# Kernel optimization log

Measured on AMD Instinct MI355X. Metric: run time of the kernel, lower is better.

Reference implementation:

```python
import jax, jax.numpy as jnp
import numpy as np

B, N, C = 8, 4096, 768
H, M = 12, 64          # num_heads, num_landmarks
D = C // H             # head_dim = 64


def setup_inputs() -> dict:
    key = jax.random.key(0)
    k1, k2, k3, k4 = jax.random.split(key, 4)
    s = 0.02
    return {
        "x": jax.random.normal(k1, (B, N, C), dtype=jnp.float32),
        "w_qkv": jax.random.normal(k2, (3 * C, C), dtype=jnp.float32) * s,
        "w_proj": jax.random.normal(k3, (C, C), dtype=jnp.float32) * s,
        "b_proj": jax.random.normal(k4, (C,), dtype=jnp.float32) * s,
    }


def iterative_inv(mat, n_iter=6):
    # mat: [B, H, M, M]; Newton-Schulz cubic iteration for pseudo-inverse
    I = jnp.eye(mat.shape[-1], dtype=mat.dtype)
    K = mat
    # init: K^T / max_j(sum_i K_ij)  per (B,H)
    scale = jnp.max(jnp.sum(K, axis=-2), axis=-1)[:, :, None, None]
    V = jnp.swapaxes(K, -1, -2) / scale
    for _ in range(n_iter):
        KV = K @ V
        V = 0.25 * V @ (13.0 * I - KV @ (15.0 * I - KV @ (7.0 * I - KV)))
    return V


def reference(x, w_qkv, w_proj, b_proj):
    b, n, c = x.shape
    qkv = (x @ w_qkv.T).reshape(b, n, 3, H, D).transpose(2, 0, 3, 1, 4)  # [3,B,H,N,D]
    Q, K, V = qkv[0], qkv[1], qkv[2]
    Q = Q / (D ** 0.5)
    # landmark pooling (N % M == 0 path): segment means of length N//M
    Kl = K.reshape(b, H, M, n // M, D).mean(axis=-2)  # [B,H,M,D]
    Ql = Q.reshape(b, H, M, n // M, D).mean(axis=-2)  # [B,H,M,D]
    kernel1 = jax.nn.softmax(jnp.einsum('bhnd,bhmd->bhnm', Q, Kl), axis=-1)   # [B,H,N,M]
    kernel2 = jax.nn.softmax(jnp.einsum('bhmd,bhld->bhml', Ql, Kl), axis=-1)  # [B,H,M,M]
    kernel3 = jax.nn.softmax(jnp.einsum('bhmd,bhnd->bhmn', Ql, K), axis=-1)   # [B,H,M,N]
    SV = (kernel1 @ iterative_inv(kernel2)) @ (kernel3 @ V)  # [B,H,N,D]
    SV = SV.transpose(0, 2, 1, 3).reshape(b, n, c)
    out = SV @ w_proj.T + b_proj
    out = out + V.transpose(0, 2, 1, 3).reshape(b, n, c)
    return out
```

## Files before the change

kernel.cpp:

```cpp
#include <hip/hip_runtime.h>
#include <hip/hip_bf16.h>
#include <stdint.h>

typedef __bf16 bf16;
typedef __bf16 bf16x8 __attribute__((ext_vector_type(8)));
typedef __bf16 bf16x4 __attribute__((ext_vector_type(4)));
typedef float f32x4 __attribute__((ext_vector_type(4)));

#define B_ 8
#define N_ 4096
#define C_ 768
#define H_ 12
#define M_ 64
#define D_ 64
#define NT_ 32768
#define C3_ 2304

typedef __attribute__((address_space(3))) void lds_void_t;
typedef const __attribute__((address_space(1))) void gvoid_t;

__device__ __forceinline__ void gl_lds16(const void* gsrc, void* ldst) {
  __builtin_amdgcn_global_load_lds((gvoid_t*)(uintptr_t)gsrc,
                                   (lds_void_t*)(uintptr_t)ldst, 16, 0, 0);
}

__device__ __forceinline__ f32x4 mfma16(bf16x8 a, bf16x8 b, f32x4 c) {
  return __builtin_amdgcn_mfma_f32_16x16x32_bf16(a, b, c, 0, 0, 0);
}

#define VMW8 asm volatile("s_waitcnt vmcnt(8)" ::: "memory")
#define VMW4 asm volatile("s_waitcnt vmcnt(4)" ::: "memory")
#define VMW0 asm volatile("s_waitcnt vmcnt(0)" ::: "memory")
#define RAWBAR() { __builtin_amdgcn_sched_barrier(0); __builtin_amdgcn_s_barrier(); __builtin_amdgcn_sched_barrier(0); }

__global__ void k_cvt(const float* __restrict__ in, bf16* __restrict__ out, int n4) {
  const int stride = gridDim.x * blockDim.x;
  for (int i = blockIdx.x * blockDim.x + threadIdx.x; i < n4; i += stride) {
    f32x4 v = *(const f32x4*)(in + (size_t)i * 4);
    bf16x4 o;
    o[0] = (bf16)v[0]; o[1] = (bf16)v[1]; o[2] = (bf16)v[2]; o[3] = (bf16)v[3];
    *(bf16x4*)(out + (size_t)i * 4) = o;
  }
}

__global__ __launch_bounds__(512, 2) void k_qkv(
    const bf16* __restrict__ xbf, const bf16* __restrict__ wbf,
    bf16* __restrict__ Qb, bf16* __restrict__ Kb, bf16* __restrict__ Vb,
    float* __restrict__ Qlf, float* __restrict__ Klf)
{
  __shared__ bf16 As[4][8192];
  __shared__ bf16 Bs[4][8192];
  const int t = threadIdx.x;
  const int wave = t >> 6, lane = t & 63;
  const int l15 = lane & 15, l16 = lane >> 4;

  const int bid = blockIdx.x;
  const int swz = (bid & 7) * 144 + (bid >> 3);
  const int bt = swz / 9, ct = swz % 9;
  const int row0 = bt * 256, col0 = ct * 256;
  const int wr = wave >> 2, wc = wave & 3;

  const int srow = t >> 2;
  const int scol = (((t & 3) ^ ((t >> 3) & 3)) << 3);
  const bf16* gaBase = xbf + (size_t)(row0 + srow) * C_ + scol;
  const bf16* gbBase = wbf + (size_t)(col0 + srow) * C_ + scol;

  const int aoff = (wr * 128 + l15) * 32 + ((l16 ^ ((l15 >> 1) & 3)) << 3);
  const int boff = (wc * 64 + l15) * 32 + ((l16 ^ ((l15 >> 1) & 3)) << 3);

  f32x4 acc[8][4] = {};

#define QSTAGE(kt3) {                                                            \
    const int sb_ = (kt3) & 3;                                                   \
    gl_lds16(gaBase + (kt3) * 32, &As[sb_][t * 8]);                              \
    gl_lds16(gbBase + (kt3) * 32, &Bs[sb_][t * 8]);                              \
    gl_lds16(gaBase + (size_t)128 * C_ + (kt3) * 32, &As[sb_][(t + 512) * 8]);   \
    gl_lds16(gbBase + (size_t)128 * C_ + (kt3) * 32, &Bs[sb_][(t + 512) * 8]); }

#define QKSTEP(kt, DO_STAGE, VMW_, DO_SYNC) {                                    \
    const bf16* as_ = As[(kt) & 3];                                              \
    const bf16* bs_ = Bs[(kt) & 3];                                              \
    bf16x8 bfr[4], afr[8];                                                       \
    _Pragma("unroll")                                                            \
    for (int j = 0; j < 4; ++j) bfr[j] = *(const bf16x8*)&bs_[boff + j * 512];   \
    _Pragma("unroll")                                                            \
    for (int i = 0; i < 8; ++i) afr[i] = *(const bf16x8*)&as_[aoff + i * 512];   \
    if (DO_STAGE) QSTAGE((kt) + 3);                                              \
    if (DO_SYNC) RAWBAR();                 \
    __builtin_amdgcn_s_setprio(1);                                               \
    _Pragma("unroll")                                                            \
    for (int i = 0; i < 8; ++i)                                                  \
      _Pragma("unroll")                                                          \
      for (int j = 0; j < 4; ++j)                                                \
        acc[i][j] = mfma16(afr[i], bfr[j], acc[i][j]);                           \
    __builtin_amdgcn_s_setprio(0);                                               \
    if (DO_SYNC) { VMW_; RAWBAR(); } }

  QSTAGE(0); QSTAGE(1); QSTAGE(2);
  VMW8;
  RAWBAR();

#pragma unroll 3
  for (int kt = 0; kt < 21; ++kt) { QKSTEP(kt, 1, VMW8, 1); }
  QKSTEP(21, 0, VMW4, 1);
  QKSTEP(22, 0, VMW0, 1);
  QKSTEP(23, 0, (void)0, 0);

#undef QKSTEP
#undef QSTAGE

  const int colblock = col0 + wc * 64;
  const int which = colblock / C_;
  const int h = (colblock % C_) / D_;
  const int b = row0 >> 12;
  const int n_base = (row0 & (N_ - 1)) + wr * 128;
  bf16* dst = (which == 0) ? Qb : (which == 1) ? Kb : Vb;
  const float scale = (which == 0) ? 0.125f : 1.0f;
  const size_t base = ((size_t)(b * H_ + h) * N_ + n_base) * D_;
#pragma unroll
  for (int i = 0; i < 8; ++i)
#pragma unroll
    for (int q = 0; q < 4; ++q) {
      const int rloc = i * 16 + l16 * 4 + q;
#pragma unroll
      for (int j = 0; j < 4; ++j) {
        const int d = j * 16 + l15;
        dst[base + (size_t)rloc * D_ + d] = (bf16)(acc[i][j][q] * scale);
      }
    }
  if (which < 2) {
    float* lmout = (which == 0) ? Qlf : Klf;
#pragma unroll
    for (int g = 0; g < 2; ++g) {
      const int m = (n_base >> 6) + g;
#pragma unroll
      for (int j = 0; j < 4; ++j) {
        float s = 0.f;
#pragma unroll
        for (int i = 4 * g; i < 4 * g + 4; ++i)
#pragma unroll
          for (int q = 0; q < 4; ++q) s += acc[i][j][q];
        s *= scale;
        s += __shfl_xor(s, 16);
        s += __shfl_xor(s, 32);
        if (l16 == 0)
          lmout[((size_t)(b * H_ + h) * M_ + m) * D_ + j * 16 + lane] = s * (1.0f / 64.0f);
      }
    }
  }
}

__global__ __launch_bounds__(512, 1) void k_inv(
    const float* __restrict__ Qlf, const float* __restrict__ Klf,
    float* __restrict__ pinv, bf16* __restrict__ Qlb, bf16* __restrict__ Klb)
{
  __shared__ float K2[4096];
  __shared__ float Vm[4096];
  __shared__ float KV[4096];
  __shared__ float T1[4096];
  __shared__ float U1[4096];
  __shared__ float tmp64[64];
  __shared__ float sscale;
  const int t = threadIdx.x;
  const int bh = blockIdx.x;
  const size_t off = (size_t)bh * 4096;
  for (int idx = t; idx < 4096; idx += 512) {
    const float q = Qlf[off + idx];
    T1[idx] = q;
    Qlb[off + idx] = (bf16)q;
  }
  for (int idx = t; idx < 4096; idx += 512) {
    const int r = idx >> 6, c = idx & 63;
    const float k = Klf[off + idx];
    U1[c * 64 + r] = k;
    Klb[off + idx] = (bf16)k;
  }
  __syncthreads();
  const int j0 = (t & 15) * 4;
  const int i0 = (t >> 4) * 2;

  auto MMstep = [&](const float* A, const float* Bm, float* O, float dg, float sg, float al) {
    float r2[2][4] = {};
    for (int k = 0; k < 64; ++k) {
      f32x4 bv = *(const f32x4*)&Bm[k * 64 + j0];
      const float a0 = A[(i0 + 0) * 64 + k];
      const float a1 = A[(i0 + 1) * 64 + k];
#pragma unroll
      for (int jj = 0; jj < 4; ++jj) { r2[0][jj] += a0 * bv[jj]; r2[1][jj] += a1 * bv[jj]; }
    }
#pragma unroll
    for (int ii = 0; ii < 2; ++ii)
#pragma unroll
      for (int jj = 0; jj < 4; ++jj)
        O[(i0 + ii) * 64 + j0 + jj] = al * (dg * A[(i0 + ii) * 64 + (j0 + jj)] + sg * r2[ii][jj]);
    __syncthreads();
  };

  {
    float r2[2][4] = {};
    for (int k = 0; k < 64; ++k) {
      f32x4 bv = *(const f32x4*)&U1[k * 64 + j0];
      const float a0 = T1[(i0 + 0) * 64 + k];
      const float a1 = T1[(i0 + 1) * 64 + k];
#pragma unroll
      for (int jj = 0; jj < 4; ++jj) { r2[0][jj] += a0 * bv[jj]; r2[1][jj] += a1 * bv[jj]; }
    }
#pragma unroll
    for (int ii = 0; ii < 2; ++ii)
#pragma unroll
      for (int jj = 0; jj < 4; ++jj)
        K2[(i0 + ii) * 64 + j0 + jj] = __expf(r2[ii][jj]);
  }
  __syncthreads();
  if (t < 64) {
    float s = 0.f;
    for (int k = 0; k < 64; ++k) s += K2[t * 64 + k];
    tmp64[t] = 1.0f / s;
  }
  __syncthreads();
  for (int idx = t; idx < 4096; idx += 512) K2[idx] *= tmp64[idx >> 6];
  __syncthreads();
  if (t < 64) {
    float s = 0.f;
    for (int i = 0; i < 64; ++i) s += K2[i * 64 + t];
    tmp64[t] = s;
  }
  __syncthreads();
  if (t == 0) {
    float mx = tmp64[0];
    for (int j2 = 1; j2 < 64; ++j2) mx = fmaxf(mx, tmp64[j2]);
    sscale = 1.0f / mx;
  }
  __syncthreads();
  for (int idx = t; idx < 4096; idx += 512) {
    const int r = idx >> 6, c = idx & 63;
    Vm[idx] = K2[c * 64 + r] * sscale;
  }
  __syncthreads();

  float* pV = Vm;
  float* pT = T1;
  for (int it = 0; it < 6; ++it) {
    MMstep(K2, pV, KV, 0.f, 1.f, 1.f);
    MMstep(KV, KV, pT, 7.f, -1.f, 1.f);
    MMstep(KV, pT, U1, 15.f, -1.f, 1.f);
    MMstep(pV, U1, pT, 13.f, -1.f, 0.25f);
    float* sw = pV; pV = pT; pT = sw;
  }
  for (int idx = t; idx < 4096; idx += 512) pinv[off + idx] = pV[idx];
}

__global__ __launch_bounds__(256, 2) void k_k3v(
    const bf16* __restrict__ Qlb, const bf16* __restrict__ Kb, const bf16* __restrict__ Vb,
    float* __restrict__ Zacc, float* __restrict__ rowsum_g)
{
  __shared__ bf16 Qls[64 * 64];
  __shared__ bf16 Ks[128 * 64];
  __shared__ bf16 Vs[128 * 64];
  __shared__ bf16 Ps[64 * 128];
  __shared__ float rs[64];
  const int t = threadIdx.x, wave = t >> 6, lane = t & 63;
  const int bh = blockIdx.x >> 3;
  const int chunk = blockIdx.x & 7;
  const size_t kvbase = (size_t)bh * N_ * D_ + (size_t)chunk * 512 * D_;
  {
    const bf16* g = Qlb + (size_t)bh * 4096;
    gl_lds16(g + t * 8, &Qls[t * 8]);
    gl_lds16(g + (t + 256) * 8, &Qls[(t + 256) * 8]);
  }
  if (t < 64) rs[t] = 0.f;
  f32x4 z[4] = {};
  for (int st = 0; st < 4; ++st) {
    const bf16* gk = Kb + kvbase + (size_t)st * 128 * D_;
    const bf16* gv = Vb + kvbase + (size_t)st * 128 * D_;
#pragma unroll
    for (int c = 0; c < 4; ++c) {
      gl_lds16(gk + (t + c * 256) * 8, &Ks[(t + c * 256) * 8]);
      gl_lds16(gv + (t + c * 256) * 8, &Vs[(t + c * 256) * 8]);
    }
    __syncthreads();
    f32x4 sacc[4][2] = {};
#pragma unroll
    for (int kk = 0; kk < 2; ++kk) {
      bf16x8 af[4], bk[2];
#pragma unroll
      for (int i = 0; i < 4; ++i)
        af[i] = *(const bf16x8*)&Qls[(i * 16 + (lane & 15)) * 64 + kk * 32 + 8 * (lane >> 4)];
#pragma unroll
      for (int j2 = 0; j2 < 2; ++j2)
        bk[j2] = *(const bf16x8*)&Ks[(wave * 32 + j2 * 16 + (lane & 15)) * 64 + kk * 32 + 8 * (lane >> 4)];
#pragma unroll
      for (int i = 0; i < 4; ++i)
#pragma unroll
        for (int j2 = 0; j2 < 2; ++j2)
          sacc[i][j2] = mfma16(af[i], bk[j2], sacc[i][j2]);
    }
#pragma unroll
    for (int i = 0; i < 4; ++i)
#pragma unroll
      for (int q = 0; q < 4; ++q) {
        const float e0 = __expf(sacc[i][0][q]);
        const float e1 = __expf(sacc[i][1][q]);
        const int m = i * 16 + (lane >> 4) * 4 + q;
        Ps[m * 128 + wave * 32 + (lane & 15)] = (bf16)e0;
        Ps[m * 128 + wave * 32 + 16 + (lane & 15)] = (bf16)e1;
        float p = e0 + e1;
        p += __shfl_xor(p, 1); p += __shfl_xor(p, 2);
        p += __shfl_xor(p, 4); p += __shfl_xor(p, 8);
        if ((lane & 15) == 0) atomicAdd(&rs[m], p);
      }
    __syncthreads();
#pragma unroll
    for (int kk = 0; kk < 4; ++kk) {
      const int kbase = kk * 32 + 8 * (lane >> 4);
      const int d = wave * 16 + (lane & 15);
      bf16x8 bv;
#pragma unroll
      for (int e = 0; e < 8; ++e) bv[e] = Vs[(kbase + e) * 64 + d];
#pragma unroll
      for (int i = 0; i < 4; ++i) {
        bf16x8 ap = *(const bf16x8*)&Ps[(i * 16 + (lane & 15)) * 128 + kbase];
        z[i] = mfma16(ap, bv, z[i]);
      }
    }
    __syncthreads();
  }
  const size_t zbase = (size_t)bh * 4096;
#pragma unroll
  for (int i = 0; i < 4; ++i)
#pragma unroll
    for (int q = 0; q < 4; ++q) {
      const int m = i * 16 + (lane >> 4) * 4 + q;
      const int d = wave * 16 + (lane & 15);
      atomicAdd(&Zacc[zbase + m * 64 + d], z[i][q]);
    }
  if (t < 64) atomicAdd(&rowsum_g[bh * 64 + t], rs[t]);
}

__global__ __launch_bounds__(256, 1) void k_comb(
    const float* __restrict__ pinv, const float* __restrict__ Zacc,
    const float* __restrict__ rowsum_g, bf16* __restrict__ Wtb)
{
  __shared__ float Pv[4096];
  __shared__ float Zn[4096];
  const int t = threadIdx.x, bh = blockIdx.x;
  const size_t off = (size_t)bh * 4096;
  for (int idx = t; idx < 4096; idx += 256) Pv[idx] = pinv[off + idx];
  for (int idx = t; idx < 4096; idx += 256)
    Zn[idx] = Zacc[off + idx] / rowsum_g[bh * 64 + (idx >> 6)];
  __syncthreads();
  const int j0 = (t & 15) * 4, i0 = (t >> 4) * 4;
  float r[4][4] = {{0.f}};
  for (int k = 0; k < 64; ++k) {
    f32x4 bv = *(const f32x4*)&Zn[k * 64 + j0];
    float a[4];
#pragma unroll
    for (int ii = 0; ii < 4; ++ii) a[ii] = Pv[(i0 + ii) * 64 + k];
#pragma unroll
    for (int ii = 0; ii < 4; ++ii)
#pragma unroll
      for (int jj = 0; jj < 4; ++jj) r[ii][jj] += a[ii] * bv[jj];
  }
#pragma unroll
  for (int ii = 0; ii < 4; ++ii)
#pragma unroll
    for (int jj = 0; jj < 4; ++jj)
      Wtb[off + (size_t)(j0 + jj) * 64 + (i0 + ii)] = (bf16)r[ii][jj];
}

__global__ __launch_bounds__(256, 2) void k_sv(
    const bf16* __restrict__ Qb, const bf16* __restrict__ Klb,
    const bf16* __restrict__ Wtb, bf16* __restrict__ SVb)
{
  __shared__ bf16 Qs[128 * 64];
  __shared__ bf16 Kls[64 * 64];
  __shared__ bf16 Wts[64 * 64];
  __shared__ bf16 Ps[128 * 64];
  const int t = threadIdx.x, wave = t >> 6, lane = t & 63;
  const int bh = blockIdx.x >> 5;
  const int nt = blockIdx.x & 31;
  const int b = bh / H_, h = bh % H_;
  {
    const bf16* gq = Qb + (size_t)bh * N_ * D_ + (size_t)nt * 128 * D_;
#pragma unroll
    for (int c = 0; c < 4; ++c) gl_lds16(gq + (t + c * 256) * 8, &Qs[(t + c * 256) * 8]);
    const bf16* gkl = Klb + (size_t)bh * 4096;
    gl_lds16(gkl + t * 8, &Kls[t * 8]);
    gl_lds16(gkl + (t + 256) * 8, &Kls[(t + 256) * 8]);
    const bf16* gw = Wtb + (size_t)bh * 4096;
    gl_lds16(gw + t * 8, &Wts[t * 8]);
    gl_lds16(gw + (t + 256) * 8, &Wts[(t + 256) * 8]);
  }
  __syncthreads();
  f32x4 sacc[2][4] = {};
#pragma unroll
  for (int kk = 0; kk < 2; ++kk) {
    bf16x8 af[2], bl[4];
#pragma unroll
    for (int r = 0; r < 2; ++r)
      af[r] = *(const bf16x8*)&Qs[(wave * 32 + r * 16 + (lane & 15)) * 64 + kk * 32 + 8 * (lane >> 4)];
#pragma unroll
    for (int j = 0; j < 4; ++j)
      bl[j] = *(const bf16x8*)&Kls[(j * 16 + (lane & 15)) * 64 + kk * 32 + 8 * (lane >> 4)];
#pragma unroll
    for (int r = 0; r < 2; ++r)
#pragma unroll
      for (int j = 0; j < 4; ++j)
        sacc[r][j] = mfma16(af[r], bl[j], sacc[r][j]);
  }
#pragma unroll
  for (int r = 0; r < 2; ++r)
#pragma unroll
    for (int q = 0; q < 4; ++q) {
      float e[4]; float s = 0.f;
#pragma unroll
      for (int j = 0; j < 4; ++j) { e[j] = __expf(sacc[r][j][q]); s += e[j]; }
      s += __shfl_xor(s, 1); s += __shfl_xor(s, 2);
      s += __shfl_xor(s, 4); s += __shfl_xor(s, 8);
      const float is = 1.0f / s;
      const int row = wave * 32 + r * 16 + (lane >> 4) * 4 + q;
#pragma unroll
      for (int j = 0; j < 4; ++j)
        Ps[row * 64 + j * 16 + (lane & 15)] = (bf16)(e[j] * is);
    }
  __syncthreads();
  f32x4 oacc[2][4] = {};
#pragma unroll
  for (int kk = 0; kk < 2; ++kk) {
    bf16x8 af[2], bw[4];
#pragma unroll
    for (int r = 0; r < 2; ++r)
      af[r] = *(const bf16x8*)&Ps[(wave * 32 + r * 16 + (lane & 15)) * 64 + kk * 32 + 8 * (lane >> 4)];
#pragma unroll
    for (int j = 0; j < 4; ++j)
      bw[j] = *(const bf16x8*)&Wts[(j * 16 + (lane & 15)) * 64 + kk * 32 + 8 * (lane >> 4)];
#pragma unroll
    for (int r = 0; r < 2; ++r)
#pragma unroll
      for (int j = 0; j < 4; ++j)
        oacc[r][j] = mfma16(af[r], bw[j], oacc[r][j]);
  }
  const size_t outbase = ((size_t)b * N_ + (size_t)nt * 128) * C_ + h * 64;
#pragma unroll
  for (int r = 0; r < 2; ++r)
#pragma unroll
    for (int q = 0; q < 4; ++q) {
      const int row = wave * 32 + r * 16 + (lane >> 4) * 4 + q;
#pragma unroll
      for (int j = 0; j < 4; ++j)
        SVb[outbase + (size_t)row * C_ + j * 16 + (lane & 15)] = (bf16)(oacc[r][j][q]);
    }
}

__global__ __launch_bounds__(256, 2) void k_proj(
    const bf16* __restrict__ SVb, const bf16* __restrict__ wpb,
    const float* __restrict__ bproj, const bf16* __restrict__ Vb,
    float* __restrict__ outp)
{
  __shared__ bf16 As[4][4096];
  __shared__ bf16 Bs[4][4096];
  const int t = threadIdx.x;
  const int wave = t >> 6, lane = t & 63;
  const int l15 = lane & 15, l16 = lane >> 4;
  const int bid = blockIdx.x;
  const int swz = (bid & 7) * 192 + (bid >> 3);
  const int bt = swz / 6, ct = swz % 6;
  const int row0 = bt * 128, col0 = ct * 128;
  const int wr = wave >> 1, wc = wave & 1;

  const int srow = t >> 2;
  const int scol = (((t & 3) ^ ((t >> 3) & 3)) << 3);
  const bf16* ga = SVb + (size_t)(row0 + srow) * C_ + scol;
  const bf16* gb = wpb + (size_t)(col0 + srow) * C_ + scol;

  const int aoff = (wr * 64 + l15) * 32 + ((l16 ^ ((l15 >> 1) & 3)) << 3);
  const int boff = (wc * 64 + l15) * 32 + ((l16 ^ ((l15 >> 1) & 3)) << 3);

  f32x4 acc[4][4] = {};

#define PSTAGE(kt3) {                                                          \
    const int sb_ = (kt3) & 3;                                                 \
    gl_lds16(ga + (kt3) * 32, &As[sb_][t * 8]);                                \
    gl_lds16(gb + (kt3) * 32, &Bs[sb_][t * 8]);                                \
    gl_lds16(ga + (size_t)64 * C_ + (kt3) * 32, &As[sb_][(t + 256) * 8]);      \
    gl_lds16(gb + (size_t)64 * C_ + (kt3) * 32, &Bs[sb_][(t + 256) * 8]); }

#define PKSTEP(kt, DO_STAGE, VMW_, DO_SYNC) {                                  \
    const bf16* as_ = As[(kt) & 3];                                            \
    const bf16* bs_ = Bs[(kt) & 3];                                            \
    bf16x8 afr[4], bfr[4];                                                     \
    _Pragma("unroll")                                                          \
    for (int j = 0; j < 4; ++j) bfr[j] = *(const bf16x8*)&bs_[boff + j * 512]; \
    _Pragma("unroll")                                                          \
    for (int i = 0; i < 4; ++i) afr[i] = *(const bf16x8*)&as_[aoff + i * 512]; \
    if (DO_STAGE) PSTAGE((kt) + 3);                                            \
    if (DO_SYNC) RAWBAR();                                                     \
    __builtin_amdgcn_s_setprio(1);                                             \
    _Pragma("unroll")                                                          \
    for (int i = 0; i < 4; ++i)                                                \
      _Pragma("unroll")                                                        \
      for (int j = 0; j < 4; ++j)                                              \
        acc[i][j] = mfma16(afr[i], bfr[j], acc[i][j]);                         \
    __builtin_amdgcn_s_setprio(0);                                             \
    if (DO_SYNC) { VMW_; RAWBAR(); } }

  PSTAGE(0); PSTAGE(1); PSTAGE(2);
  VMW8;
  RAWBAR();

#pragma unroll 3
  for (int kt = 0; kt < 21; ++kt) { PKSTEP(kt, 1, VMW8, 1); }
  PKSTEP(21, 0, VMW4, 1);
  PKSTEP(22, 0, VMW0, 1);
  PKSTEP(23, 0, (void)0, 0);

#undef PKSTEP
#undef PSTAGE

#pragma unroll
  for (int i = 0; i < 4; ++i)
#pragma unroll
    for (int q = 0; q < 4; ++q) {
      const int row = row0 + wr * 64 + i * 16 + l16 * 4 + q;
      const int b = row >> 12, n = row & (N_ - 1);
#pragma unroll
      for (int j = 0; j < 4; ++j) {
        const int col = col0 + wc * 64 + j * 16 + l15;
        const int h = col >> 6, d = col & 63;
        const float v = acc[i][j][q] + bproj[col] +
                        (float)Vb[((size_t)(b * H_ + h) * N_ + n) * D_ + d];
        outp[(size_t)row * C_ + col] = v;
      }
    }
}

extern "C" void kernel_launch(void* const* d_in, const int* in_sizes, int n_in,
                              void* d_out, int out_size, void* d_ws, size_t ws_size,
                              hipStream_t stream) {
  const float* x = (const float*)d_in[0];
  const float* wqkv = (const float*)d_in[1];
  const float* wproj = (const float*)d_in[2];
  const float* bproj = (const float*)d_in[3];
  float* outp = (float*)d_out;
  char* ws = (char*)d_ws;

  size_t off = 0;
  auto take = [&](size_t bytes) { char* p = ws + off; off += bytes; return p; };
  bf16* xbf     = (bf16*)take(50331648);
  bf16* wqkvbf  = (bf16*)take(3538944);
  bf16* wprojbf = (bf16*)take(1179648);
  bf16* Qb      = (bf16*)take(50331648);
  bf16* Kb      = (bf16*)take(50331648);
  bf16* Vb      = (bf16*)take(50331648);
  float* Qlf    = (float*)take(1572864);
  float* Klf    = (float*)take(1572864);
  bf16* Qlb     = (bf16*)take(786432);
  bf16* Klb     = (bf16*)take(786432);
  float* pinvp  = (float*)take(1572864);
  float* Zacc   = (float*)take(1572864);
  float* rowsum = (float*)take(24576);
  bf16* Wtb     = (bf16*)take(786432);
  bf16* SVb     = xbf;

  hipMemsetAsync(Zacc, 0, 1572864 + 24576, stream);

  k_cvt<<<2048, 256, 0, stream>>>(x, xbf, 25165824 / 4);
  k_cvt<<<432, 256, 0, stream>>>(wqkv, wqkvbf, 1769472 / 4);
  k_cvt<<<144, 256, 0, stream>>>(wproj, wprojbf, 589824 / 4);
  k_qkv<<<1152, 512, 0, stream>>>(xbf, wqkvbf, Qb, Kb, Vb, Qlf, Klf);
  k_inv<<<96, 512, 0, stream>>>(Qlf, Klf, pinvp, Qlb, Klb);
  k_k3v<<<768, 256, 0, stream>>>(Qlb, Kb, Vb, Zacc, rowsum);
  k_comb<<<96, 256, 0, stream>>>(pinvp, Zacc, rowsum, Wtb);
  k_sv<<<96 * 32, 256, 0, stream>>>(Qb, Klb, Wtb, SVb);
  k_proj<<<1536, 256, 0, stream>>>(SVb, wprojbf, bproj, Vb, outp);
}
```

Before: 391.6 us.

## Software-pipeline LDS fragment loads with MFMA in QKV and projection GEMMs

Restructures the K-loop of both GEMM kernels so the LDS-to-register fragment loads for the next k-step are issued while the current step's MFMAs run, using double-buffered register fragments. It drops one barrier per step, relaxes the vmcnt waits, and fully unrolls the loop. The aim is to hide LDS read latency behind matrix math and cut synchronisation. In exchange it raises register pressure, which may hurt occupancy under launch_bounds(512,2). Correctness depends on the reduced barrier and wait scheme still ordering the asynchronous LDS fills safely.

```diff
diff --git a/kernel.cpp b/kernel.cpp
--- a/kernel.cpp
+++ b/kernel.cpp
@@ -57,18 +57,19 @@
   const int bid = blockIdx.x;
   const int swz = (bid & 7) * 144 + (bid >> 3);
   const int bt = swz / 9, ct = swz % 9;
-  const int row0 = bt * 256, col0 = ct * 256;
+  const int row0 = bt * 256, ct0 = ct * 256;
   const int wr = wave >> 2, wc = wave & 3;
 
   const int srow = t >> 2;
   const int scol = (((t & 3) ^ ((t >> 3) & 3)) << 3);
   const bf16* gaBase = xbf + (size_t)(row0 + srow) * C_ + scol;
-  const bf16* gbBase = wbf + (size_t)(col0 + srow) * C_ + scol;
+  const bf16* gbBase = wbf + (size_t)(ct0 + srow) * C_ + scol;
 
   const int aoff = (wr * 128 + l15) * 32 + ((l16 ^ ((l15 >> 1) & 3)) << 3);
   const int boff = (wc * 64 + l15) * 32 + ((l16 ^ ((l15 >> 1) & 3)) << 3);
 
   f32x4 acc[8][4] = {};
+  bf16x8 afr0[4], afr1[4], bfr[2][4];
 
 #define QSTAGE(kt3) {                                                            \
     const int sb_ = (kt3) & 3;                                                   \
@@ -77,39 +78,61 @@
     gl_lds16(gaBase + (size_t)128 * C_ + (kt3) * 32, &As[sb_][(t + 512) * 8]);   \
     gl_lds16(gbBase + (size_t)128 * C_ + (kt3) * 32, &Bs[sb_][(t + 512) * 8]); }
 
-#define QKSTEP(kt, DO_STAGE, VMW_, DO_SYNC) {                                    \
-    const bf16* as_ = As[(kt) & 3];                                              \
-    const bf16* bs_ = Bs[(kt) & 3];                                              \
-    bf16x8 bfr[4], afr[8];                                                       \
-    _Pragma("unroll")                                                            \
-    for (int j = 0; j < 4; ++j) bfr[j] = *(const bf16x8*)&bs_[boff + j * 512];   \
-    _Pragma("unroll")                                                            \
-    for (int i = 0; i < 8; ++i) afr[i] = *(const bf16x8*)&as_[aoff + i * 512];   \
-    if (DO_STAGE) QSTAGE((kt) + 3);                                              \
-    if (DO_SYNC) RAWBAR();                 \
+#define QKSTEP(kt, DO_STAGE, DO_NXT, VMW_, DO_BAR) {                             \
+    if (DO_STAGE) QSTAGE((kt) + 3);                                             \
+    { const bf16* asC = As[(kt) & 3];                                            \
+      _Pragma("unroll")                                                          \
+      for (int i = 0; i < 4; ++i)                                                \
+        afr1[i] = *(const bf16x8*)&asC[aoff + (4 + i) * 512]; }                  \
     __builtin_amdgcn_s_setprio(1);                                               \
     _Pragma("unroll")                                                            \
-    for (int i = 0; i < 8; ++i)                                                  \
+    for (int i = 0; i < 4; ++i)                                                  \
       _Pragma("unroll")                                                          \
       for (int j = 0; j < 4; ++j)                                                \
-        acc[i][j] = mfma16(afr[i], bfr[j], acc[i][j]);                           \
+        acc[i][j] = mfma16(afr0[i], bfr[(kt) & 1][j], acc[i][j]);                \
     __builtin_amdgcn_s_setprio(0);                                               \
-    if (DO_SYNC) { VMW_; RAWBAR(); } }
+    if (DO_NXT) {                                                                \
+      const bf16* asN = As[((kt) + 1) & 3];                                      \
+      const bf16* bsN = Bs[((kt) + 1) & 3];                                      \
+      _Pragma("unroll")                                                          \
+      for (int i = 0; i < 4; ++i)                                                \
+        afr0[i] = *(const bf16x8*)&asN[aoff + i * 512];                          \
+      _Pragma("unroll")                                                          \
+      for (int j = 0; j < 4; ++j)                                                \
+        bfr[((kt) + 1) & 1][j] = *(const bf16x8*)&bsN[boff + j * 512]; }         \
+    __builtin_amdgcn_s_setprio(1);                                               \
+    _Pragma("unroll")                                                            \
+    for (int i = 0; i < 4; ++i)                                                  \
+      _Pragma("unroll")                                                          \
+      for (int j = 0; j < 4; ++j)                                                \
+        acc[4 + i][j] = mfma16(afr1[i], bfr[(kt) & 1][j], acc[4 + i][j]);        \
+    __builtin_amdgcn_s_setprio(0);                                               \
+    VMW_;                                                                        \
+    if (DO_BAR) RAWBAR(); }
 
   QSTAGE(0); QSTAGE(1); QSTAGE(2);
-  VMW8;
+  VMW4;
   RAWBAR();
-
-#pragma unroll 3
-  for (int kt = 0; kt < 21; ++kt) { QKSTEP(kt, 1, VMW8, 1); }
-  QKSTEP(21, 0, VMW4, 1);
-  QKSTEP(22, 0, VMW0, 1);
-  QKSTEP(23, 0, (void)0, 0);
+#pragma unroll
+  for (int i = 0; i < 4; ++i) afr0[i] = *(const bf16x8*)&As[0][aoff + i * 512];
+#pragma unroll
+  for (int j = 0; j < 4; ++j) bfr[0][j] = *(const bf16x8*)&Bs[0][boff + j * 512];
+
+  QKSTEP(0, 1, 1, VMW4, 1)  QKSTEP(1, 1, 1, VMW4, 1)  QKSTEP(2, 1, 1, VMW4, 1)
+  QKSTEP(3, 1, 1, VMW4, 1)  QKSTEP(4, 1, 1, VMW4, 1)  QKSTEP(5, 1, 1, VMW4, 1)
+  QKSTEP(6, 1, 1, VMW4, 1)  QKSTEP(7, 1, 1, VMW4, 1)  QKSTEP(8, 1, 1, VMW4, 1)
+  QKSTEP(9, 1, 1, VMW4, 1)  QKSTEP(10, 1, 1, VMW4, 1) QKSTEP(11, 1, 1, VMW4, 1)
+  QKSTEP(12, 1, 1, VMW4, 1) QKSTEP(13, 1, 1, VMW4, 1) QKSTEP(14, 1, 1, VMW4, 1)
+  QKSTEP(15, 1, 1, VMW4, 1) QKSTEP(16, 1, 1, VMW4, 1) QKSTEP(17, 1, 1, VMW4, 1)
+  QKSTEP(18, 1, 1, VMW4, 1) QKSTEP(19, 1, 1, VMW4, 1) QKSTEP(20, 1, 1, VMW4, 1)
+  QKSTEP(21, 0, 1, VMW0, 1)
+  QKSTEP(22, 0, 1, (void)0, 1)
+  QKSTEP(23, 0, 0, (void)0, 0)
 
 #undef QKSTEP
 #undef QSTAGE
 
-  const int colblock = col0 + wc * 64;
+  const int colblock = ct0 + wc * 64;
   const int which = colblock / C_;
   const int h = (colblock % C_) / D_;
   const int b = row0 >> 12;
@@ -477,6 +500,7 @@
   const int boff = (wc * 64 + l15) * 32 + ((l16 ^ ((l15 >> 1) & 3)) << 3);
 
   f32x4 acc[4][4] = {};
+  bf16x8 afr[2][4], bfr[2][4];
 
 #define PSTAGE(kt3) {                                                          \
     const int sb_ = (kt3) & 3;                                                 \
@@ -485,34 +509,45 @@
     gl_lds16(ga + (size_t)64 * C_ + (kt3) * 32, &As[sb_][(t + 256) * 8]);      \
     gl_lds16(gb + (size_t)64 * C_ + (kt3) * 32, &Bs[sb_][(t + 256) * 8]); }
 
-#define PKSTEP(kt, DO_STAGE, VMW_, DO_SYNC) {                                  \
-    const bf16* as_ = As[(kt) & 3];                                            \
-    const bf16* bs_ = Bs[(kt) & 3];                                            \
-    bf16x8 afr[4], bfr[4];                                                     \
-    _Pragma("unroll")                                                          \
-    for (int j = 0; j < 4; ++j) bfr[j] = *(const bf16x8*)&bs_[boff + j * 512]; \
-    _Pragma("unroll")                                                          \
-    for (int i = 0; i < 4; ++i) afr[i] = *(const bf16x8*)&as_[aoff + i * 512]; \
+#define PKSTEP(kt, DO_STAGE, DO_NXT, VMW_, DO_BAR) {                           \
     if (DO_STAGE) PSTAGE((kt) + 3);                                            \
-    if (DO_SYNC) RAWBAR();                                                     \
+    if (DO_NXT) {                                                              \
+      const bf16* asN = As[((kt) + 1) & 3];                                    \
+      const bf16* bsN = Bs[((kt) + 1) & 3];                                    \
+      _Pragma("unroll")                                                        \
+      for (int i = 0; i < 4; ++i)                                              \
+        afr[((kt) + 1) & 1][i] = *(const bf16x8*)&asN[aoff + i * 512];         \
+      _Pragma("unroll")                                                        \
+      for (int j = 0; j < 4; ++j)                                              \
+        bfr[((kt) + 1) & 1][j] = *(const bf16x8*)&bsN[boff + j * 512]; }       \
     __builtin_amdgcn_s_setprio(1);                                             \
     _Pragma("unroll")                                                          \
     for (int i = 0; i < 4; ++i)                                                \
       _Pragma("unroll")                                                        \
       for (int j = 0; j < 4; ++j)                                              \
-        acc[i][j] = mfma16(afr[i], bfr[j], acc[i][j]);                         \
+        acc[i][j] = mfma16(afr[(kt) & 1][i], bfr[(kt) & 1][j], acc[i][j]);     \
     __builtin_amdgcn_s_setprio(0);                                             \
-    if (DO_SYNC) { VMW_; RAWBAR(); } }
+    VMW_;                                                                      \
+    if (DO_BAR) RAWBAR(); }
 
   PSTAGE(0); PSTAGE(1); PSTAGE(2);
-  VMW8;
+  VMW4;
   RAWBAR();
-
-#pragma unroll 3
-  for (int kt = 0; kt < 21; ++kt) { PKSTEP(kt, 1, VMW8, 1); }
-  PKSTEP(21, 0, VMW4, 1);
-  PKSTEP(22, 0, VMW0, 1);
-  PKSTEP(23, 0, (void)0, 0);
+#pragma unroll
+  for (int i = 0; i < 4; ++i) afr[0][i] = *(const bf16x8*)&As[0][aoff + i * 512];
+#pragma unroll
+  for (int j = 0; j < 4; ++j) bfr[0][j] = *(const bf16x8*)&Bs[0][boff + j * 512];
+
+  PKSTEP(0, 1, 1, VMW4, 1)  PKSTEP(1, 1, 1, VMW4, 1)  PKSTEP(2, 1, 1, VMW4, 1)
+  PKSTEP(3, 1, 1, VMW4, 1)  PKSTEP(4, 1, 1, VMW4, 1)  PKSTEP(5, 1, 1, VMW4, 1)
+  PKSTEP(6, 1, 1, VMW4, 1)  PKSTEP(7, 1, 1, VMW4, 1)  PKSTEP(8, 1, 1, VMW4, 1)
+  PKSTEP(9, 1, 1, VMW4, 1)  PKSTEP(10, 1, 1, VMW4, 1) PKSTEP(11, 1, 1, VMW4, 1)
+  PKSTEP(12, 1, 1, VMW4, 1) PKSTEP(13, 1, 1, VMW4, 1) PKSTEP(14, 1, 1, VMW4, 1)
+  PKSTEP(15, 1, 1, VMW4, 1) PKSTEP(16, 1, 1, VMW4, 1) PKSTEP(17, 1, 1, VMW4, 1)
+  PKSTEP(18, 1, 1, VMW4, 1) PKSTEP(19, 1, 1, VMW4, 1) PKSTEP(20, 1, 1, VMW4, 1)
+  PKSTEP(21, 0, 1, VMW0, 1)
+  PKSTEP(22, 0, 1, (void)0, 1)
+  PKSTEP(23, 0, 0, (void)0, 0)
 
 #undef PKSTEP
 #undef PSTAGE
```

After: 388.6 us. No clear change (-0.8%).
